# Optimization experiments

Measured on AMD Instinct MI355X. Metric: run time of the kernel, lower is better.

## Reference

```python
import jax, jax.numpy as jnp
import numpy as np

EPS = 1e-12  # tf.nn.l2_normalize epsilon used inside keras CosineSimilarity


def _cos(a, b):
    # keras CosineSimilarity returns -cos; callers negate explicitly.
    an = a / jnp.sqrt(jnp.maximum(jnp.sum(a * a, axis=-1, keepdims=True), EPS))
    bn = b / jnp.sqrt(jnp.maximum(jnp.sum(b * b, axis=-1, keepdims=True), EPS))
    return jnp.sum(an * bn, axis=-1)


def setup_inputs() -> dict:
    key = jax.random.key(0)
    B, S, D, H, N = 1024, 200, 128, 128, 64
    ks = jax.random.split(key, 8)
    X_series = jax.random.normal(ks[0], (B, S, D), jnp.float32)
    pos_series = jax.random.normal(ks[1], (S, D), jnp.float32)
    X_item = jax.random.normal(ks[2], (B, D), jnp.float32)
    origin = jax.random.normal(ks[3], (B, N, D), jnp.float32)  # X_negative
    # contiguous-prefix validity mask (module assumes valid positions form a prefix)
    lengths = jax.random.randint(ks[4], (B,), 1, S + 1)
    valid_mask = jnp.arange(S)[None, :] < lengths[:, None]
    # learned params (GlorotUniform-scale init)
    Wp = jax.random.normal(ks[5], (D, H), jnp.float32) * 0.08
    We = jax.random.normal(ks[6], (D, H), jnp.float32) * 0.08
    z = jax.random.normal(ks[7], (H,), jnp.float32) * 0.1
    return {"X_series": X_series, "pos_series": pos_series, "X_item": X_item,
            "valid_mask": valid_mask, "origin": origin, "Wp": Wp, "We": We, "z": z}


def reference(X_series, pos_series, X_item, valid_mask, origin, Wp, We, z):
    B, S, D = X_series.shape
    # additive tanh attention: z . tanh(X_series @ We + pos_series @ Wp)
    hidden = jnp.tanh(jnp.einsum('bsd,dh->bsh', X_series, We) + (pos_series @ Wp)[None])
    scores = jnp.einsum('bsh,h->bs', hidden, z)
    scores = jnp.where(valid_mask, scores, -jnp.inf)
    attn = jax.nn.softmax(scores, axis=-1)                      # [B,S]
    attentioned = attn[:, :, None] * X_series                    # [B,S,D]
    attention_output = jnp.sum(attentioned, axis=1)              # [B,D]
    inner = jnp.sum(attention_output * X_item, axis=-1, keepdims=True)
    concated = jnp.concatenate([attention_output, inner], axis=1)  # [B,D+1]

    # ---- auxiliary loss ----
    last_idx = jnp.sum(valid_mask.astype(jnp.int32), axis=1) - 1
    last_vec = attentioned[jnp.arange(B), last_idx]              # gather_nd
    new_mask = (jnp.arange(S)[None, :] < last_idx[:, None]).astype(X_series.dtype)
    out_vec = jnp.sum(attentioned * new_mask[:, :, None], axis=1)  # [B,D]
    # keras CosineSimilarity = -cos_sim; then mapped to (x+1)/2 and used as logits
    pos_logits = (-_cos(last_vec, out_vec) + 1.0) / 2.0          # [B]
    neg_logits = (-_cos(origin, out_vec[:, None, :]) + 1.0) / 2.0  # [B,N]
    pos_loss = jax.nn.softplus(-pos_logits)  # sigmoid_xent labels=1
    neg_loss = jax.nn.softplus(neg_logits)   # sigmoid_xent labels=0
    # NB: TF reduces pos_loss over its only axis -> scalar, broadcast-added to [B]
    auxiliary_loss = jnp.sum(pos_loss) + jnp.sum(neg_loss, axis=-1)  # [B]
    return concated, auxiliary_loss
```

## Files before the change

kernel.cpp:

```cpp
#include <hip/hip_runtime.h>
#include <hip/hip_bf16.h>
#include <math.h>

#define B_ 1024
#define S_ 200
#define D_ 128
#define H_ 128
#define N_ 64
#define SP_ 208

typedef __attribute__((ext_vector_type(8))) short short8;
typedef __attribute__((ext_vector_type(8))) __bf16 bf16x8;
typedef __attribute__((ext_vector_type(4))) float floatx4;

typedef __attribute__((address_space(1))) void gvoid_t;
typedef __attribute__((address_space(3))) void lvoid_t;

static __device__ __forceinline__ float bf2f(unsigned short u) {
    union { unsigned int i; float f; } v; v.i = ((unsigned int)u) << 16; return v.f;
}
static __device__ __forceinline__ unsigned short f2bf(float f) {
    union { float f; unsigned int u; } v; v.f = f;
    unsigned int u = v.u;
    return (unsigned short)((u + 0x7FFFu + ((u >> 16) & 1u)) >> 16);
}
static __device__ __forceinline__ float ld1(const void* p, int isbf, size_t i) {
    return isbf ? bf2f(((const unsigned short*)p)[i]) : ((const float*)p)[i];
}
static __device__ __forceinline__ float fast_tanh(float x) {
    float t = __expf(2.0f * x);
    return 1.0f - 2.0f * __builtin_amdgcn_rcpf(t + 1.0f);
}
static __device__ __forceinline__ void gload_lds16(const void* g, void* l) {
    __builtin_amdgcn_global_load_lds((const gvoid_t*)g, (lvoid_t*)l, 16, 0, 0);
}

static __device__ __forceinline__ int detect_wave_256(const void* p) {
    int lane = threadIdx.x & 63;
    uint4 w = ((const uint4*)p)[lane];
    unsigned int ws[4] = {w.x, w.y, w.z, w.w};
    int pass = 0;
#pragma unroll
    for (int k = 0; k < 4; ++k) {
        unsigned int e = (ws[k] >> 7) & 0xFF;
        pass += (e == 0 || (e >= 96 && e <= 140)) ? 1 : 0;
    }
#pragma unroll
    for (int off = 32; off; off >>= 1) pass += __shfl_xor(pass, off, 64);
    return pass * 4 >= 256 * 3;
}
static __device__ __forceinline__ int detect_wave_64(const void* p) {
    int lane = threadIdx.x & 63;
    unsigned int w = ((const unsigned int*)p)[lane];
    unsigned int e = (w >> 7) & 0xFF;
    int pass = (e == 0 || (e >= 96 && e <= 140)) ? 1 : 0;
#pragma unroll
    for (int off = 32; off; off >>= 1) pass += __shfl_xor(pass, off, 64);
    return pass * 4 >= 64 * 3;
}
static __device__ __forceinline__ int detect_mask_u8(const void* p) {
    int lane = threadIdx.x & 63;
    uint4 w = ((const uint4*)p)[lane];
    unsigned int x = (w.x | w.y | w.z | w.w) & 0xFFFFFF00u;
    return (__ballot(x != 0) != 0ULL) ? 1 : 0;
}

__global__ __launch_bounds__(128) void prep_kernel(
    const void* __restrict__ We, const void* __restrict__ pos,
    const void* __restrict__ Wp,
    unsigned short* __restrict__ WeTf, float* __restrict__ pbL)
{
    int blk = blockIdx.x, t = threadIdx.x;
    __shared__ unsigned short T[128][136];
    __shared__ float prow[D_];
    __shared__ int fl[2];
    if (blk == 0) {
        if (t < 64) { int f = detect_wave_256(We); if (t == 0) fl[0] = f; }
        __syncthreads();
        int fWe = fl[0];
        for (int c = t; c < 2048; c += 128) {
            int d = c >> 4, h8 = (c & 15) * 8;
            short8 v;
            if (fWe) {
                v = *(const short8*)((const unsigned short*)We + d * H_ + h8);
            } else {
                const float* p = (const float*)We + d * H_ + h8;
                float4 a = ((const float4*)p)[0], b = ((const float4*)p)[1];
                v[0] = (short)f2bf(a.x); v[1] = (short)f2bf(a.y);
                v[2] = (short)f2bf(a.z); v[3] = (short)f2bf(a.w);
                v[4] = (short)f2bf(b.x); v[5] = (short)f2bf(b.y);
                v[6] = (short)f2bf(b.z); v[7] = (short)f2bf(b.w);
            }
            *(short8*)(&T[d][h8]) = v;
        }
        __syncthreads();
        for (int i = t; i < 2048; i += 128) {
            int frag = i >> 6, ln = i & 63;
            int nt = frag >> 2, kks = frag & 3;
            int h = nt * 16 + (ln & 15);
            int dbase = kks * 32 + (ln >> 4) * 8;
            short8 v;
#pragma unroll
            for (int j = 0; j < 8; ++j) v[j] = (short)T[dbase + j][h];
            *(short8*)(WeTf + (size_t)i * 8) = v;
        }
    } else {
        if (t < 64)       { int f = detect_wave_256(pos); if (t == 0)  fl[0] = f; }
        else if (t < 128) { int f = detect_wave_256(Wp);  if (t == 64) fl[1] = f; }
        __syncthreads();
        int fPos = fl[0], fWp = fl[1];
        int s = blk - 1, h = t;
        prow[h] = ld1(pos, fPos, (size_t)s * D_ + h);
        __syncthreads();
        float acc = 0.f;
        if (fWp) {
            const unsigned short* W = (const unsigned short*)Wp;
            for (int d = 0; d < D_; ++d) acc = fmaf(prow[d], bf2f(W[d * H_ + h]), acc);
        } else {
            const float* W = (const float*)Wp;
            for (int d = 0; d < D_; ++d) acc = fmaf(prow[d], W[d * H_ + h], acc);
        }
        int mt = s >> 4, qr = s & 15;
        int idx = (((mt * 8 + (h >> 4)) * 64 + (qr >> 2) * 16 + (h & 15)) << 2) + (qr & 3);
        pbL[idx] = acc;
    }
}

__global__ __launch_bounds__(512, 4) void fused_kernel(
    const void* __restrict__ Xs, const void* __restrict__ Xitem,
    const void* __restrict__ maskv, const void* __restrict__ origin,
    const unsigned short* __restrict__ WeTf, const float* __restrict__ pbL,
    const void* __restrict__ zv,
    float* __restrict__ pos_loss, float* __restrict__ neg_sum,
    float* __restrict__ out)
{
    int b = blockIdx.x, t = threadIdx.x;
    int wv = t >> 6, lane = t & 63;
    int quad = lane >> 4, mrow = lane & 15;

    __shared__ __align__(16) unsigned short Xsh[SP_ * D_];
    __shared__ __align__(16) float partial[4096];
    __shared__ float red4[512];
    __shared__ float attn[256];
    __shared__ float outv[D_];
    __shared__ float red[32];
    __shared__ int redi[8];

    int fXs = detect_wave_256(Xs);
    int fXi = detect_wave_256(Xitem);
    int fOr = detect_wave_256(origin);
    int fz  = detect_wave_64(zv);
    int fMk = detect_mask_u8(maskv);

    if (fXs) {
        const unsigned short* gb = (const unsigned short*)Xs + (size_t)b * (S_ * D_);
        for (int i = t; i < S_ * 16; i += 512) {
            int s = i >> 4, c8 = (i & 15) * 8;
            int cs = c8 ^ ((s & 7) << 3);
            gload_lds16(gb + (size_t)s * D_ + cs, Xsh + (size_t)i * 8);
        }
    } else {
        const float* gb = (const float*)Xs + (size_t)b * (S_ * D_);
        for (int i = t; i < S_ * 16; i += 512) {
            int s = i >> 4, c8 = (i & 15) * 8;
            const float* p = gb + (size_t)s * D_ + c8;
            float4 a = ((const float4*)p)[0], c = ((const float4*)p)[1];
            short8 v;
            v[0] = (short)f2bf(a.x); v[1] = (short)f2bf(a.y);
            v[2] = (short)f2bf(a.z); v[3] = (short)f2bf(a.w);
            v[4] = (short)f2bf(c.x); v[5] = (short)f2bf(c.y);
            v[6] = (short)f2bf(c.z); v[7] = (short)f2bf(c.w);
            *(short8*)(Xsh + s * D_ + (c8 ^ ((s & 7) << 3))) = v;
        }
    }

    int nn = t >> 3, part = t & 7;
    float o_f[16];
    if (fOr) {
        const unsigned short* p = (const unsigned short*)origin + ((size_t)b * N_ + nn) * D_ + part * 16;
#pragma unroll
        for (int j = 0; j < 2; ++j) {
            uint4 u = *(const uint4*)(p + j * 8);
            o_f[j*8+0] = bf2f((unsigned short)(u.x & 0xffff));
            o_f[j*8+1] = bf2f((unsigned short)(u.x >> 16));
            o_f[j*8+2] = bf2f((unsigned short)(u.y & 0xffff));
            o_f[j*8+3] = bf2f((unsigned short)(u.y >> 16));
            o_f[j*8+4] = bf2f((unsigned short)(u.z & 0xffff));
            o_f[j*8+5] = bf2f((unsigned short)(u.z >> 16));
            o_f[j*8+6] = bf2f((unsigned short)(u.w & 0xffff));
            o_f[j*8+7] = bf2f((unsigned short)(u.w >> 16));
        }
    } else {
        const float* p = (const float*)origin + ((size_t)b * N_ + nn) * D_ + part * 16;
#pragma unroll
        for (int j = 0; j < 4; ++j) {
            float4 v = *(const float4*)(p + j * 4);
            o_f[j*4+0] = v.x; o_f[j*4+1] = v.y; o_f[j*4+2] = v.z; o_f[j*4+3] = v.w;
        }
    }
    float xiv = (t < D_) ? ld1(Xitem, fXi, (size_t)b * D_ + t) : 0.f;
    int nz = 0;
    if (t < S_)
        nz = fMk ? (((const unsigned char*)maskv)[(size_t)b * S_ + t] != 0)
                 : (((const int*)maskv)[(size_t)b * S_ + t] != 0);

    int nt = wv;
    bf16x8 bfr[4];
#pragma unroll
    for (int kks = 0; kks < 4; ++kks)
        bfr[kks] = __builtin_bit_cast(bf16x8,
            *(const short8*)(WeTf + (size_t)((((nt << 2) + kks) << 6) + lane) * 8));
    float zl = ld1(zv, fz, nt * 16 + mrow);
    const float4* pbw = (const float4*)pbL + nt * 64 + lane;
    float4 pbc = pbw[0];

    asm volatile("s_waitcnt vmcnt(0)" ::: "memory");
    __syncthreads();

    float* sp = partial;
    for (int mt = 0; mt < 13; ++mt) {
        float4 pbn = pbc;
        if (mt < 12) pbn = pbw[(size_t)(mt + 1) * 512];
        floatx4 acc = {0.f, 0.f, 0.f, 0.f};
        int r = mt * 16 + mrow;
        int rbase = r * D_, rx = (r & 7) << 3;
#pragma unroll
        for (int kks = 0; kks < 4; ++kks) {
            bf16x8 af = __builtin_bit_cast(bf16x8,
                *(const short8*)(Xsh + rbase + ((kks * 32 + quad * 8) ^ rx)));
            acc = __builtin_amdgcn_mfma_f32_16x16x32_bf16(af, bfr[kks], acc, 0, 0, 0);
        }
#pragma unroll
        for (int reg = 0; reg < 4; ++reg) {
            float val = fast_tanh(acc[reg] + (&pbc.x)[reg]) * zl;
            val += __shfl_xor(val, 1, 64);
            val += __shfl_xor(val, 2, 64);
            val += __shfl_xor(val, 4, 64);
            val += __shfl_xor(val, 8, 64);
            int s = mt * 16 + quad * 4 + reg;
            if (mrow == 0 && s < S_) sp[nt * SP_ + s] = val;
        }
        pbc = pbn;
    }
    __syncthreads();

    float myscore = -INFINITY;
    if (t < S_) {
        float ss = 0.f;
#pragma unroll
        for (int w8 = 0; w8 < 8; ++w8) ss += sp[w8 * SP_ + t];
        myscore = ss;
    }
    unsigned long long bal = __ballot(nz);
    float scv = nz ? myscore : -INFINITY;
    float m = scv;
#pragma unroll
    for (int off = 32; off; off >>= 1) m = fmaxf(m, __shfl_xor(m, off, 64));
    if (lane == 0) { red[wv] = m; redi[wv] = __popcll(bal); }
    __syncthreads();
    int length = redi[0] + redi[1] + redi[2] + redi[3]
               + redi[4] + redi[5] + redi[6] + redi[7];
    int last = length - 1;
    float mglob = red[0];
#pragma unroll
    for (int i = 1; i < 8; ++i) mglob = fmaxf(mglob, red[i]);
    float e = nz ? expf(myscore - mglob) : 0.f;
    float rr = e;
#pragma unroll
    for (int off = 32; off; off >>= 1) rr += __shfl_xor(rr, off, 64);
    if (lane == 0) red[8 + wv] = rr;
    __syncthreads();
    float ssum = red[8] + red[9] + red[10] + red[11]
               + red[12] + red[13] + red[14] + red[15];
    if (t < 256) attn[t] = e / ssum;
    __syncthreads();

    {
        int spi = t >> 4;
        int d8 = (t & 15) * 8;
        float a0 = 0.f, a1 = 0.f, a2 = 0.f, a3 = 0.f;
        float a4 = 0.f, a5 = 0.f, a6 = 0.f, a7 = 0.f;
        for (int s = spi; s < S_; s += 32) {
            float ww = attn[s];
            short8 v2 = *(const short8*)(Xsh + s * D_ + (d8 ^ ((s & 7) << 3)));
            a0 = fmaf(ww, bf2f((unsigned short)v2[0]), a0);
            a1 = fmaf(ww, bf2f((unsigned short)v2[1]), a1);
            a2 = fmaf(ww, bf2f((unsigned short)v2[2]), a2);
            a3 = fmaf(ww, bf2f((unsigned short)v2[3]), a3);
            a4 = fmaf(ww, bf2f((unsigned short)v2[4]), a4);
            a5 = fmaf(ww, bf2f((unsigned short)v2[5]), a5);
            a6 = fmaf(ww, bf2f((unsigned short)v2[6]), a6);
            a7 = fmaf(ww, bf2f((unsigned short)v2[7]), a7);
        }
        float4 w0 = {a0, a1, a2, a3}, w1 = {a4, a5, a6, a7};
        *(float4*)(partial + spi * D_ + d8)     = w0;
        *(float4*)(partial + spi * D_ + d8 + 4) = w1;
    }
    __syncthreads();
    {
        int g = t >> 7, d = t & 127;
        float sgp = 0.f;
#pragma unroll
        for (int p = 0; p < 8; ++p) sgp += partial[(g * 8 + p) * D_ + d];
        red4[g * D_ + d] = sgp;
    }
    __syncthreads();

    if (t < D_) {
        float att = red4[t] + red4[D_ + t] + red4[2 * D_ + t] + red4[3 * D_ + t];
        float xl = bf2f(Xsh[last * D_ + (t ^ ((last & 7) << 3))]);
        float lv = attn[last] * xl;
        float ov = att - lv;
        outv[t] = ov;
        out[(size_t)b * (D_ + 1) + t] = att;
        float r0 = att * xiv;
        float r1 = lv * lv, r2 = lv * ov, r3 = ov * ov;
#pragma unroll
        for (int off = 32; off; off >>= 1) {
            r0 += __shfl_xor(r0, off, 64);
            r1 += __shfl_xor(r1, off, 64);
            r2 += __shfl_xor(r2, off, 64);
            r3 += __shfl_xor(r3, off, 64);
        }
        if (lane == 0) { red[wv] = r0; red[8 + wv] = r1; red[16 + wv] = r2; red[24 + wv] = r3; }
    }
    __syncthreads();
    float vv = red[24] + red[25];
    if (t == 0) {
        out[(size_t)b * (D_ + 1) + D_] = red[0] + red[1];
        float ll = red[8] + red[9], lo = red[16] + red[17];
        float cosv = lo / (sqrtf(fmaxf(ll, 1e-12f)) * sqrtf(fmaxf(vv, 1e-12f)));
        float pl = 0.5f * (1.f - cosv);
        pos_loss[b] = log1pf(expf(-pl));
    }

    {
        float* p_oo = partial;
        float* p_ov = partial + 512;
        float o_oo = 0.f, o_ov = 0.f;
#pragma unroll
        for (int j = 0; j < 16; ++j) {
            float wv_ = outv[part * 16 + j];
            o_oo = fmaf(o_f[j], o_f[j], o_oo);
            o_ov = fmaf(o_f[j], wv_, o_ov);
        }
        p_oo[part * 64 + nn] = o_oo;
        p_ov[part * 64 + nn] = o_ov;
        __syncthreads();
        if (t < 64) {
            float oo = 0.f, ov2 = 0.f;
#pragma unroll
            for (int p8 = 0; p8 < 8; ++p8) { oo += p_oo[p8 * 64 + t]; ov2 += p_ov[p8 * 64 + t]; }
            float cosn = ov2 / (sqrtf(fmaxf(oo, 1e-12f)) * sqrtf(fmaxf(vv, 1e-12f)));
            float nl = 0.5f * (1.f - cosn);
            float nloss = log1pf(expf(nl));
#pragma unroll
            for (int off = 32; off; off >>= 1) nloss += __shfl_xor(nloss, off, 64);
            if (t == 0) neg_sum[b] = nloss;
        }
    }
}

__global__ __launch_bounds__(1024) void final_kernel(
    const float* __restrict__ pos_loss,
    const float* __restrict__ neg_sum,
    float* __restrict__ out)
{
    __shared__ float red[16];
    int t = threadIdx.x;
    float v = pos_loss[t];
    for (int off = 32; off; off >>= 1) v += __shfl_xor(v, off, 64);
    if ((t & 63) == 0) red[t >> 6] = v;
    __syncthreads();
    if (t == 0) {
        float s = 0.f;
#pragma unroll
        for (int i = 0; i < 16; ++i) s += red[i];
        red[0] = s;
    }
    __syncthreads();
    out[(size_t)B_ * (D_ + 1) + t] = red[0] + neg_sum[t];
}

extern "C" void kernel_launch(void* const* d_in, const int* in_sizes, int n_in,
                              void* d_out, int out_size, void* d_ws, size_t ws_size,
                              hipStream_t stream) {
    const void* Xs     = d_in[0];
    const void* pos    = d_in[1];
    const void* Xitem  = d_in[2];
    const void* mask   = d_in[3];
    const void* origin = d_in[4];
    const void* Wp     = d_in[5];
    const void* We     = d_in[6];
    const void* zv     = d_in[7];

    unsigned short* WeTf = (unsigned short*)d_ws;
    float* pbL      = (float*)((char*)d_ws + 32768);
    float* pos_loss = pbL + 13 * 8 * 64 * 4;
    float* neg_sum  = pos_loss + B_;
    float* out = (float*)d_out;

    prep_kernel<<<201, 128, 0, stream>>>(We, pos, Wp, WeTf, pbL);
    fused_kernel<<<B_, 512, 0, stream>>>(Xs, Xitem, mask, origin, WeTf, pbL, zv,
                                         pos_loss, neg_sum, out);
    final_kernel<<<1, 1024, 0, stream>>>(pos_loss, neg_sum, out);
}
```

Before: 236.5 us.

## Process one batch row per wave with online softmax and streamed X loads

Restructures the fused kernel so that each 64-lane wave handles a whole batch row, with four rows per 256-thread block, in place of one 512-thread block per row. X_series is no longer staged in LDS; MFMA A-fragments are loaded straight from global memory and prefetched one tile ahead. The attention softmax and weighted sum are computed in a single streaming pass using a flash-style running max and rescaling. This removes the block-wide syncs and the large LDS footprint. In exchange, each wave now does all 8 H-tiles of MFMA work and re-reads X rows from global or cache for the weighted sum. The prep kernel also zero-fills the padded pbL entries so the bias can seed the accumulators directly.

```diff
diff --git a/kernel.cpp b/kernel.cpp
--- a/kernel.cpp
+++ b/kernel.cpp
@@ -7,7 +7,6 @@
 #define D_ 128
 #define H_ 128
 #define N_ 64
-#define SP_ 208
 
 typedef __attribute__((ext_vector_type(8))) short short8;
 typedef __attribute__((ext_vector_type(8))) __bf16 bf16x8;
@@ -104,6 +103,11 @@
             for (int j = 0; j < 8; ++j) v[j] = (short)T[dbase + j][h];
             *(short8*)(WeTf + (size_t)i * 8) = v;
         }
+        for (int i = t; i < 1024; i += 128) {
+            int nt = i >> 7, j = i & 127;
+            int q = 2 + (j >> 6), m = (j >> 2) & 15, r = j & 3;
+            pbL[(((96 + nt) * 64 + q * 16 + m) << 2) + r] = 0.f;
+        }
     } else {
         if (t < 64)       { int f = detect_wave_256(pos); if (t == 0)  fl[0] = f; }
         else if (t < 128) { int f = detect_wave_256(Wp);  if (t == 64) fl[1] = f; }
@@ -126,7 +130,7 @@
     }
 }
 
-__global__ __launch_bounds__(512, 4) void fused_kernel(
+__global__ __launch_bounds__(256, 4) void fused_kernel(
     const void* __restrict__ Xs, const void* __restrict__ Xitem,
     const void* __restrict__ maskv, const void* __restrict__ origin,
     const unsigned short* __restrict__ WeTf, const float* __restrict__ pbL,
@@ -134,17 +138,14 @@
     float* __restrict__ pos_loss, float* __restrict__ neg_sum,
     float* __restrict__ out)
 {
-    int b = blockIdx.x, t = threadIdx.x;
+    int t = threadIdx.x;
     int wv = t >> 6, lane = t & 63;
     int quad = lane >> 4, mrow = lane & 15;
-
-    __shared__ __align__(16) unsigned short Xsh[SP_ * D_];
-    __shared__ __align__(16) float partial[4096];
-    __shared__ float red4[512];
-    __shared__ float attn[256];
-    __shared__ float outv[D_];
-    __shared__ float red[32];
-    __shared__ int redi[8];
+    int b = blockIdx.x * 4 + wv;
+    int d0 = lane * 2;
+
+    __shared__ __align__(16) unsigned short WeSh[16384];
+    __shared__ __align__(16) float outbuf[4 * D_];
 
     int fXs = detect_wave_256(Xs);
     int fXi = detect_wave_256(Xitem);
@@ -152,213 +153,274 @@
     int fz  = detect_wave_64(zv);
     int fMk = detect_mask_u8(maskv);
 
-    if (fXs) {
-        const unsigned short* gb = (const unsigned short*)Xs + (size_t)b * (S_ * D_);
-        for (int i = t; i < S_ * 16; i += 512) {
-            int s = i >> 4, c8 = (i & 15) * 8;
-            int cs = c8 ^ ((s & 7) << 3);
-            gload_lds16(gb + (size_t)s * D_ + cs, Xsh + (size_t)i * 8);
-        }
+    for (int i = t; i < 2048; i += 256)
+        gload_lds16(WeTf + (size_t)i * 8, WeSh + (size_t)i * 8);
+
+    const unsigned short* Xg16 = (const unsigned short*)Xs + (size_t)b * S_ * D_;
+    const float*          Xg32 = (const float*)Xs + (size_t)b * S_ * D_;
+
+    int len = 0;
+    {
+#pragma unroll
+        for (int k = 0; k < 4; ++k) {
+            int s = lane + 64 * k;
+            int nzv = 0;
+            if (s < S_)
+                nzv = fMk ? (((const unsigned char*)maskv)[(size_t)b * S_ + s] != 0)
+                          : (((const int*)maskv)[(size_t)b * S_ + s] != 0);
+            len += __popcll(__ballot(nzv));
+        }
+    }
+    int last = len - 1;
+    float zr[8];
+#pragma unroll
+    for (int nt = 0; nt < 8; ++nt) zr[nt] = ld1(zv, fz, nt * 16 + mrow);
+    float xi0, xi1;
+    if (fXi) {
+        unsigned int u = *(const unsigned int*)((const unsigned short*)Xitem + (size_t)b * D_ + d0);
+        xi0 = bf2f((unsigned short)(u & 0xffff)); xi1 = bf2f((unsigned short)(u >> 16));
     } else {
-        const float* gb = (const float*)Xs + (size_t)b * (S_ * D_);
-        for (int i = t; i < S_ * 16; i += 512) {
-            int s = i >> 4, c8 = (i & 15) * 8;
-            const float* p = gb + (size_t)s * D_ + c8;
-            float4 a = ((const float4*)p)[0], c = ((const float4*)p)[1];
-            short8 v;
-            v[0] = (short)f2bf(a.x); v[1] = (short)f2bf(a.y);
-            v[2] = (short)f2bf(a.z); v[3] = (short)f2bf(a.w);
-            v[4] = (short)f2bf(c.x); v[5] = (short)f2bf(c.y);
-            v[6] = (short)f2bf(c.z); v[7] = (short)f2bf(c.w);
-            *(short8*)(Xsh + s * D_ + (c8 ^ ((s & 7) << 3))) = v;
-        }
-    }
-
-    int nn = t >> 3, part = t & 7;
-    float o_f[16];
-    if (fOr) {
-        const unsigned short* p = (const unsigned short*)origin + ((size_t)b * N_ + nn) * D_ + part * 16;
-#pragma unroll
-        for (int j = 0; j < 2; ++j) {
-            uint4 u = *(const uint4*)(p + j * 8);
-            o_f[j*8+0] = bf2f((unsigned short)(u.x & 0xffff));
-            o_f[j*8+1] = bf2f((unsigned short)(u.x >> 16));
-            o_f[j*8+2] = bf2f((unsigned short)(u.y & 0xffff));
-            o_f[j*8+3] = bf2f((unsigned short)(u.y >> 16));
-            o_f[j*8+4] = bf2f((unsigned short)(u.z & 0xffff));
-            o_f[j*8+5] = bf2f((unsigned short)(u.z >> 16));
-            o_f[j*8+6] = bf2f((unsigned short)(u.w & 0xffff));
-            o_f[j*8+7] = bf2f((unsigned short)(u.w >> 16));
-        }
-    } else {
-        const float* p = (const float*)origin + ((size_t)b * N_ + nn) * D_ + part * 16;
-#pragma unroll
-        for (int j = 0; j < 4; ++j) {
-            float4 v = *(const float4*)(p + j * 4);
-            o_f[j*4+0] = v.x; o_f[j*4+1] = v.y; o_f[j*4+2] = v.z; o_f[j*4+3] = v.w;
-        }
-    }
-    float xiv = (t < D_) ? ld1(Xitem, fXi, (size_t)b * D_ + t) : 0.f;
-    int nz = 0;
-    if (t < S_)
-        nz = fMk ? (((const unsigned char*)maskv)[(size_t)b * S_ + t] != 0)
-                 : (((const int*)maskv)[(size_t)b * S_ + t] != 0);
-
-    int nt = wv;
-    bf16x8 bfr[4];
-#pragma unroll
-    for (int kks = 0; kks < 4; ++kks)
-        bfr[kks] = __builtin_bit_cast(bf16x8,
-            *(const short8*)(WeTf + (size_t)((((nt << 2) + kks) << 6) + lane) * 8));
-    float zl = ld1(zv, fz, nt * 16 + mrow);
-    const float4* pbw = (const float4*)pbL + nt * 64 + lane;
-    float4 pbc = pbw[0];
+        float2 v = *(const float2*)((const float*)Xitem + (size_t)b * D_ + d0);
+        xi0 = v.x; xi1 = v.y;
+    }
 
     asm volatile("s_waitcnt vmcnt(0)" ::: "memory");
     __syncthreads();
 
-    float* sp = partial;
+#define LOADA(MT, AF)                                                              \
+    {                                                                              \
+        int r_ = (MT) * 16 + mrow; if (r_ > 199) r_ = 199;                         \
+        if (fXs) {                                                                 \
+            const unsigned short* p_ = Xg16 + (size_t)r_ * D_ + quad * 8;          \
+            _Pragma("unroll")                                                      \
+            for (int kk_ = 0; kk_ < 4; ++kk_)                                      \
+                AF[kk_] = __builtin_bit_cast(bf16x8, *(const short8*)(p_ + kk_ * 32)); \
+        } else {                                                                   \
+            const float* p_ = Xg32 + (size_t)r_ * D_ + quad * 8;                   \
+            _Pragma("unroll")                                                      \
+            for (int kk_ = 0; kk_ < 4; ++kk_) {                                    \
+                float4 a_ = ((const float4*)(p_ + kk_ * 32))[0];                   \
+                float4 b2_ = ((const float4*)(p_ + kk_ * 32))[1];                  \
+                short8 v_;                                                         \
+                v_[0] = (short)f2bf(a_.x); v_[1] = (short)f2bf(a_.y);              \
+                v_[2] = (short)f2bf(a_.z); v_[3] = (short)f2bf(a_.w);              \
+                v_[4] = (short)f2bf(b2_.x); v_[5] = (short)f2bf(b2_.y);            \
+                v_[6] = (short)f2bf(b2_.z); v_[7] = (short)f2bf(b2_.w);            \
+                AF[kk_] = __builtin_bit_cast(bf16x8, v_);                          \
+            }                                                                      \
+        }                                                                          \
+    }
+
+#define LOADXP(R, X0, X1)                                                          \
+    {                                                                              \
+        if (fXs) {                                                                 \
+            unsigned int u_ = *(const unsigned int*)(Xg16 + (size_t)(R) * D_ + d0);\
+            X0 = bf2f((unsigned short)(u_ & 0xffff));                              \
+            X1 = bf2f((unsigned short)(u_ >> 16));                                 \
+        } else {                                                                   \
+            float2 v_ = *(const float2*)(Xg32 + (size_t)(R) * D_ + d0);            \
+            X0 = v_.x; X1 = v_.y;                                                  \
+        }                                                                          \
+    }
+
+    bf16x8 afc[4], afn[4];
+    LOADA(0, afc);
+
+    float m_run = -INFINITY, l_run = 0.f;
+    float O0 = 0.f, O1 = 0.f;
+    float slv = -INFINITY;
+    float dsc = 0.f;
+    float de0 = 0.f, de1 = 0.f, de2 = 0.f, de3 = 0.f;
+    int dmt = 0;
+    const float4* pb4 = (const float4*)pbL;
+
     for (int mt = 0; mt < 13; ++mt) {
-        float4 pbn = pbc;
-        if (mt < 12) pbn = pbw[(size_t)(mt + 1) * 512];
-        floatx4 acc = {0.f, 0.f, 0.f, 0.f};
-        int r = mt * 16 + mrow;
-        int rbase = r * D_, rx = (r & 7) << 3;
+        float4 pbt[8];
+#pragma unroll
+        for (int nt = 0; nt < 8; ++nt)
+            pbt[nt] = pb4[(size_t)(mt * 8 + nt) * 64 + lane];
+        if (mt < 12) LOADA(mt + 1, afn);
+
+        if (mt > 0) {
+            O0 *= dsc; O1 *= dsc;
+#pragma unroll
+            for (int q = 0; q < 4; ++q) {
+                float eq0 = q ? __shfl_xor(de0, q << 4, 64) : de0;
+                float eq1 = q ? __shfl_xor(de1, q << 4, 64) : de1;
+                float eq2 = q ? __shfl_xor(de2, q << 4, 64) : de2;
+                float eq3 = q ? __shfl_xor(de3, q << 4, 64) : de3;
+                int rb = (dmt << 4) + ((quad ^ q) << 2);
+#pragma unroll
+                for (int r = 0; r < 4; ++r) {
+                    float es = (r == 0) ? eq0 : (r == 1) ? eq1 : (r == 2) ? eq2 : eq3;
+                    int row = rb + r; if (row > 199) row = 199;
+                    float x0, x1; LOADXP(row, x0, x1);
+                    O0 = fmaf(es, x0, O0);
+                    O1 = fmaf(es, x1, O1);
+                }
+            }
+        }
+
+        floatx4 acc[8];
+#pragma unroll
+        for (int nt = 0; nt < 8; ++nt) {
+            acc[nt][0] = pbt[nt].x; acc[nt][1] = pbt[nt].y;
+            acc[nt][2] = pbt[nt].z; acc[nt][3] = pbt[nt].w;
+        }
 #pragma unroll
         for (int kks = 0; kks < 4; ++kks) {
-            bf16x8 af = __builtin_bit_cast(bf16x8,
-                *(const short8*)(Xsh + rbase + ((kks * 32 + quad * 8) ^ rx)));
-            acc = __builtin_amdgcn_mfma_f32_16x16x32_bf16(af, bfr[kks], acc, 0, 0, 0);
-        }
-#pragma unroll
-        for (int reg = 0; reg < 4; ++reg) {
-            float val = fast_tanh(acc[reg] + (&pbc.x)[reg]) * zl;
-            val += __shfl_xor(val, 1, 64);
-            val += __shfl_xor(val, 2, 64);
-            val += __shfl_xor(val, 4, 64);
-            val += __shfl_xor(val, 8, 64);
-            int s = mt * 16 + quad * 4 + reg;
-            if (mrow == 0 && s < S_) sp[nt * SP_ + s] = val;
-        }
-        pbc = pbn;
-    }
-    __syncthreads();
-
-    float myscore = -INFINITY;
-    if (t < S_) {
-        float ss = 0.f;
-#pragma unroll
-        for (int w8 = 0; w8 < 8; ++w8) ss += sp[w8 * SP_ + t];
-        myscore = ss;
-    }
-    unsigned long long bal = __ballot(nz);
-    float scv = nz ? myscore : -INFINITY;
-    float m = scv;
-#pragma unroll
-    for (int off = 32; off; off >>= 1) m = fmaxf(m, __shfl_xor(m, off, 64));
-    if (lane == 0) { red[wv] = m; redi[wv] = __popcll(bal); }
-    __syncthreads();
-    int length = redi[0] + redi[1] + redi[2] + redi[3]
-               + redi[4] + redi[5] + redi[6] + redi[7];
-    int last = length - 1;
-    float mglob = red[0];
-#pragma unroll
-    for (int i = 1; i < 8; ++i) mglob = fmaxf(mglob, red[i]);
-    float e = nz ? expf(myscore - mglob) : 0.f;
-    float rr = e;
-#pragma unroll
-    for (int off = 32; off; off >>= 1) rr += __shfl_xor(rr, off, 64);
-    if (lane == 0) red[8 + wv] = rr;
-    __syncthreads();
-    float ssum = red[8] + red[9] + red[10] + red[11]
-               + red[12] + red[13] + red[14] + red[15];
-    if (t < 256) attn[t] = e / ssum;
-    __syncthreads();
+#pragma unroll
+            for (int nt = 0; nt < 8; ++nt) {
+                short8 bv = *(const short8*)(WeSh + (size_t)(((nt << 2) + kks) * 64 + lane) * 8);
+                acc[nt] = __builtin_amdgcn_mfma_f32_16x16x32_bf16(
+                    afc[kks], __builtin_bit_cast(bf16x8, bv), acc[nt], 0, 0, 0);
+            }
+        }
+
+        float val0, val1, val2, val3;
+#pragma unroll
+        for (int r = 0; r < 4; ++r) {
+            float v = 0.f;
+#pragma unroll
+            for (int nt = 0; nt < 8; ++nt)
+                v = fmaf(fast_tanh(acc[nt][r]), zr[nt], v);
+            v += __shfl_xor(v, 1, 64);
+            v += __shfl_xor(v, 2, 64);
+            v += __shfl_xor(v, 4, 64);
+            v += __shfl_xor(v, 8, 64);
+            if (r == 0) val0 = v; else if (r == 1) val1 = v;
+            else if (r == 2) val2 = v; else val3 = v;
+        }
+
+        int sbase = (mt << 4) + (quad << 2);
+        float x0m = (sbase + 0 < len) ? val0 : -INFINITY;
+        float x1m = (sbase + 1 < len) ? val1 : -INFINITY;
+        float x2m = (sbase + 2 < len) ? val2 : -INFINITY;
+        float x3m = (sbase + 3 < len) ? val3 : -INFINITY;
+        if (sbase + 0 == last) slv = val0;
+        if (sbase + 1 == last) slv = val1;
+        if (sbase + 2 == last) slv = val2;
+        if (sbase + 3 == last) slv = val3;
+        float tm = fmaxf(fmaxf(x0m, x1m), fmaxf(x2m, x3m));
+        tm = fmaxf(tm, __shfl_xor(tm, 16, 64));
+        tm = fmaxf(tm, __shfl_xor(tm, 32, 64));
+        float mn = fmaxf(m_run, tm);
+        float sc_ = __expf(m_run - mn);
+        de0 = (sbase + 0 < len) ? __expf(val0 - mn) : 0.f;
+        de1 = (sbase + 1 < len) ? __expf(val1 - mn) : 0.f;
+        de2 = (sbase + 2 < len) ? __expf(val2 - mn) : 0.f;
+        de3 = (sbase + 3 < len) ? __expf(val3 - mn) : 0.f;
+        float tl = de0 + de1 + de2 + de3;
+        tl += __shfl_xor(tl, 16, 64);
+        tl += __shfl_xor(tl, 32, 64);
+        l_run = l_run * sc_ + tl;
+        m_run = mn;
+        dsc = sc_; dmt = mt;
+
+#pragma unroll
+        for (int kks = 0; kks < 4; ++kks) afc[kks] = afn[kks];
+    }
 
     {
-        int spi = t >> 4;
-        int d8 = (t & 15) * 8;
-        float a0 = 0.f, a1 = 0.f, a2 = 0.f, a3 = 0.f;
-        float a4 = 0.f, a5 = 0.f, a6 = 0.f, a7 = 0.f;
-        for (int s = spi; s < S_; s += 32) {
-            float ww = attn[s];
-            short8 v2 = *(const short8*)(Xsh + s * D_ + (d8 ^ ((s & 7) << 3)));
-            a0 = fmaf(ww, bf2f((unsigned short)v2[0]), a0);
-            a1 = fmaf(ww, bf2f((unsigned short)v2[1]), a1);
-            a2 = fmaf(ww, bf2f((unsigned short)v2[2]), a2);
-            a3 = fmaf(ww, bf2f((unsigned short)v2[3]), a3);
-            a4 = fmaf(ww, bf2f((unsigned short)v2[4]), a4);
-            a5 = fmaf(ww, bf2f((unsigned short)v2[5]), a5);
-            a6 = fmaf(ww, bf2f((unsigned short)v2[6]), a6);
-            a7 = fmaf(ww, bf2f((unsigned short)v2[7]), a7);
-        }
-        float4 w0 = {a0, a1, a2, a3}, w1 = {a4, a5, a6, a7};
-        *(float4*)(partial + spi * D_ + d8)     = w0;
-        *(float4*)(partial + spi * D_ + d8 + 4) = w1;
-    }
-    __syncthreads();
-    {
-        int g = t >> 7, d = t & 127;
-        float sgp = 0.f;
-#pragma unroll
-        for (int p = 0; p < 8; ++p) sgp += partial[(g * 8 + p) * D_ + d];
-        red4[g * D_ + d] = sgp;
-    }
-    __syncthreads();
-
-    if (t < D_) {
-        float att = red4[t] + red4[D_ + t] + red4[2 * D_ + t] + red4[3 * D_ + t];
-        float xl = bf2f(Xsh[last * D_ + (t ^ ((last & 7) << 3))]);
-        float lv = attn[last] * xl;
-        float ov = att - lv;
-        outv[t] = ov;
-        out[(size_t)b * (D_ + 1) + t] = att;
-        float r0 = att * xiv;
-        float r1 = lv * lv, r2 = lv * ov, r3 = ov * ov;
-#pragma unroll
-        for (int off = 32; off; off >>= 1) {
-            r0 += __shfl_xor(r0, off, 64);
-            r1 += __shfl_xor(r1, off, 64);
-            r2 += __shfl_xor(r2, off, 64);
-            r3 += __shfl_xor(r3, off, 64);
-        }
-        if (lane == 0) { red[wv] = r0; red[8 + wv] = r1; red[16 + wv] = r2; red[24 + wv] = r3; }
-    }
-    __syncthreads();
-    float vv = red[24] + red[25];
-    if (t == 0) {
-        out[(size_t)b * (D_ + 1) + D_] = red[0] + red[1];
-        float ll = red[8] + red[9], lo = red[16] + red[17];
-        float cosv = lo / (sqrtf(fmaxf(ll, 1e-12f)) * sqrtf(fmaxf(vv, 1e-12f)));
+        O0 *= dsc; O1 *= dsc;
+#pragma unroll
+        for (int q = 0; q < 4; ++q) {
+            float eq0 = q ? __shfl_xor(de0, q << 4, 64) : de0;
+            float eq1 = q ? __shfl_xor(de1, q << 4, 64) : de1;
+            float eq2 = q ? __shfl_xor(de2, q << 4, 64) : de2;
+            float eq3 = q ? __shfl_xor(de3, q << 4, 64) : de3;
+            int rb = (12 << 4) + ((quad ^ q) << 2);
+#pragma unroll
+            for (int r = 0; r < 4; ++r) {
+                float es = (r == 0) ? eq0 : (r == 1) ? eq1 : (r == 2) ? eq2 : eq3;
+                int row = rb + r; if (row > 199) row = 199;
+                float x0, x1; LOADXP(row, x0, x1);
+                O0 = fmaf(es, x0, O0);
+                O1 = fmaf(es, x1, O1);
+            }
+        }
+    }
+
+    float att0 = O0 / l_run, att1 = O1 / l_run;
+    slv = fmaxf(slv, __shfl_xor(slv, 16, 64));
+    slv = fmaxf(slv, __shfl_xor(slv, 32, 64));
+    float al = __expf(slv - m_run) / l_run;
+    float xl0, xl1; LOADXP(last, xl0, xl1);
+    float lv0 = al * xl0, lv1 = al * xl1;
+    float ov0 = att0 - lv0, ov1 = att1 - lv1;
+    float* outw = outbuf + wv * D_;
+    outw[d0] = ov0; outw[d0 + 1] = ov1;
+
+    float r0 = att0 * xi0 + att1 * xi1;
+    float r1 = lv0 * lv0 + lv1 * lv1;
+    float r2 = lv0 * ov0 + lv1 * ov1;
+    float r3 = ov0 * ov0 + ov1 * ov1;
+#pragma unroll
+    for (int off = 32; off; off >>= 1) {
+        r0 += __shfl_xor(r0, off, 64);
+        r1 += __shfl_xor(r1, off, 64);
+        r2 += __shfl_xor(r2, off, 64);
+        r3 += __shfl_xor(r3, off, 64);
+    }
+    out[(size_t)b * (D_ + 1) + d0] = att0;
+    out[(size_t)b * (D_ + 1) + d0 + 1] = att1;
+    if (lane == 0) {
+        out[(size_t)b * (D_ + 1) + D_] = r0;
+        float cosv = r2 / (sqrtf(fmaxf(r1, 1e-12f)) * sqrtf(fmaxf(r3, 1e-12f)));
         float pl = 0.5f * (1.f - cosv);
         pos_loss[b] = log1pf(expf(-pl));
     }
+    float vv = r3;
 
     {
-        float* p_oo = partial;
-        float* p_ov = partial + 512;
-        float o_oo = 0.f, o_ov = 0.f;
-#pragma unroll
-        for (int j = 0; j < 16; ++j) {
-            float wv_ = outv[part * 16 + j];
-            o_oo = fmaf(o_f[j], o_f[j], o_oo);
-            o_ov = fmaf(o_f[j], wv_, o_ov);
-        }
-        p_oo[part * 64 + nn] = o_oo;
-        p_ov[part * 64 + nn] = o_ov;
-        __syncthreads();
-        if (t < 64) {
-            float oo = 0.f, ov2 = 0.f;
-#pragma unroll
-            for (int p8 = 0; p8 < 8; ++p8) { oo += p_oo[p8 * 64 + t]; ov2 += p_ov[p8 * 64 + t]; }
-            float cosn = ov2 / (sqrtf(fmaxf(oo, 1e-12f)) * sqrtf(fmaxf(vv, 1e-12f)));
-            float nl = 0.5f * (1.f - cosn);
-            float nloss = log1pf(expf(nl));
-#pragma unroll
-            for (int off = 32; off; off >>= 1) nloss += __shfl_xor(nloss, off, 64);
-            if (t == 0) neg_sum[b] = nloss;
-        }
-    }
+        float oo = 0.f, ovd = 0.f;
+        if (fOr) {
+            const unsigned short* orow = (const unsigned short*)origin + ((size_t)b * N_ + lane) * D_;
+#pragma unroll 4
+            for (int j = 0; j < 16; ++j) {
+                short8 og = *(const short8*)(orow + j * 8);
+                float4 c0 = *(const float4*)(outw + j * 8);
+                float4 c1 = *(const float4*)(outw + j * 8 + 4);
+                float f0 = bf2f((unsigned short)og[0]), f1 = bf2f((unsigned short)og[1]);
+                float f2 = bf2f((unsigned short)og[2]), f3 = bf2f((unsigned short)og[3]);
+                float f4 = bf2f((unsigned short)og[4]), f5 = bf2f((unsigned short)og[5]);
+                float f6 = bf2f((unsigned short)og[6]), f7 = bf2f((unsigned short)og[7]);
+                oo  = fmaf(f0, f0, oo);  ovd = fmaf(f0, c0.x, ovd);
+                oo  = fmaf(f1, f1, oo);  ovd = fmaf(f1, c0.y, ovd);
+                oo  = fmaf(f2, f2, oo);  ovd = fmaf(f2, c0.z, ovd);
+                oo  = fmaf(f3, f3, oo);  ovd = fmaf(f3, c0.w, ovd);
+                oo  = fmaf(f4, f4, oo);  ovd = fmaf(f4, c1.x, ovd);
+                oo  = fmaf(f5, f5, oo);  ovd = fmaf(f5, c1.y, ovd);
+                oo  = fmaf(f6, f6, oo);  ovd = fmaf(f6, c1.z, ovd);
+                oo  = fmaf(f7, f7, oo);  ovd = fmaf(f7, c1.w, ovd);
+            }
+        } else {
+            const float* orow = (const float*)origin + ((size_t)b * N_ + lane) * D_;
+#pragma unroll 4
+            for (int j = 0; j < 16; ++j) {
+                float4 g0 = *(const float4*)(orow + j * 8);
+                float4 g1 = *(const float4*)(orow + j * 8 + 4);
+                float4 c0 = *(const float4*)(outw + j * 8);
+                float4 c1 = *(const float4*)(outw + j * 8 + 4);
+                oo  = fmaf(g0.x, g0.x, oo);  ovd = fmaf(g0.x, c0.x, ovd);
+                oo  = fmaf(g0.y, g0.y, oo);  ovd = fmaf(g0.y, c0.y, ovd);
+                oo  = fmaf(g0.z, g0.z, oo);  ovd = fmaf(g0.z, c0.z, ovd);
+                oo  = fmaf(g0.w, g0.w, oo);  ovd = fmaf(g0.w, c0.w, ovd);
+                oo  = fmaf(g1.x, g1.x, oo);  ovd = fmaf(g1.x, c1.x, ovd);
+                oo  = fmaf(g1.y, g1.y, oo);  ovd = fmaf(g1.y, c1.y, ovd);
+                oo  = fmaf(g1.z, g1.z, oo);  ovd = fmaf(g1.z, c1.z, ovd);
+                oo  = fmaf(g1.w, g1.w, oo);  ovd = fmaf(g1.w, c1.w, ovd);
+            }
+        }
+        float cosn = ovd / (sqrtf(fmaxf(oo, 1e-12f)) * sqrtf(fmaxf(vv, 1e-12f)));
+        float nl = 0.5f * (1.f - cosn);
+        float nloss = log1pf(expf(nl));
+#pragma unroll
+        for (int off = 32; off; off >>= 1) nloss += __shfl_xor(nloss, off, 64);
+        if (lane == 0) neg_sum[b] = nloss;
+    }
+#undef LOADA
+#undef LOADXP
 }
 
 __global__ __launch_bounds__(1024) void final_kernel(
@@ -401,7 +463,7 @@
     float* out = (float*)d_out;
 
     prep_kernel<<<201, 128, 0, stream>>>(We, pos, Wp, WeTf, pbL);
-    fused_kernel<<<B_, 512, 0, stream>>>(Xs, Xitem, mask, origin, WeTf, pbL, zv,
-                                         pos_loss, neg_sum, out);
+    fused_kernel<<<B_ / 4, 256, 0, stream>>>(Xs, Xitem, mask, origin, WeTf, pbL, zv,
+                                             pos_loss, neg_sum, out);
     final_kernel<<<1, 1024, 0, stream>>>(pos_loss, neg_sum, out);
 }
```

Measured after the change: 428.7 us. 1.81x slower.

## Drop LDS staging of X_series, stream MFMA operands from global to raise occupancy

Applied to the files above, without the earlier changes.

Removes the 53KB shared-memory copy of each batch's X_series. MFMA A-fragments are now loaded straight from global memory with one-tile register double-buffering, and the weighted-sum pass re-reads X from global (expected to hit in cache). This shrinks LDS use so launch bounds can request 6 blocks per CU instead of 4. It also computes the sequence length up front via ballot, moves the softmax into a single wave, folds the positional bias into the MFMA accumulator init, and zero-pads the bias tail in the prep kernel. The cost is a second global read of X and possibly more register pressure.

```diff
diff --git a/kernel.cpp b/kernel.cpp
--- a/kernel.cpp
+++ b/kernel.cpp
@@ -7,14 +7,10 @@
 #define D_ 128
 #define H_ 128
 #define N_ 64
-#define SP_ 208
 
 typedef __attribute__((ext_vector_type(8))) short short8;
 typedef __attribute__((ext_vector_type(8))) __bf16 bf16x8;
 typedef __attribute__((ext_vector_type(4))) float floatx4;
-
-typedef __attribute__((address_space(1))) void gvoid_t;
-typedef __attribute__((address_space(3))) void lvoid_t;
 
 static __device__ __forceinline__ float bf2f(unsigned short u) {
     union { unsigned int i; float f; } v; v.i = ((unsigned int)u) << 16; return v.f;
@@ -30,9 +26,6 @@
 static __device__ __forceinline__ float fast_tanh(float x) {
     float t = __expf(2.0f * x);
     return 1.0f - 2.0f * __builtin_amdgcn_rcpf(t + 1.0f);
-}
-static __device__ __forceinline__ void gload_lds16(const void* g, void* l) {
-    __builtin_amdgcn_global_load_lds((const gvoid_t*)g, (lvoid_t*)l, 16, 0, 0);
 }
 
 static __device__ __forceinline__ int detect_wave_256(const void* p) {
@@ -104,6 +97,11 @@
             for (int j = 0; j < 8; ++j) v[j] = (short)T[dbase + j][h];
             *(short8*)(WeTf + (size_t)i * 8) = v;
         }
+        for (int i = t; i < 1024; i += 128) {
+            int nt = i >> 7, j = i & 127;
+            int q = 2 + (j >> 6), m = (j >> 2) & 15, r = j & 3;
+            pbL[(((96 + nt) * 64 + q * 16 + m) << 2) + r] = 0.f;
+        }
     } else {
         if (t < 64)       { int f = detect_wave_256(pos); if (t == 0)  fl[0] = f; }
         else if (t < 128) { int f = detect_wave_256(Wp);  if (t == 64) fl[1] = f; }
@@ -126,7 +124,7 @@
     }
 }
 
-__global__ __launch_bounds__(512, 4) void fused_kernel(
+__global__ __launch_bounds__(512, 6) void fused_kernel(
     const void* __restrict__ Xs, const void* __restrict__ Xitem,
     const void* __restrict__ maskv, const void* __restrict__ origin,
     const unsigned short* __restrict__ WeTf, const float* __restrict__ pbL,
@@ -138,13 +136,10 @@
     int wv = t >> 6, lane = t & 63;
     int quad = lane >> 4, mrow = lane & 15;
 
-    __shared__ __align__(16) unsigned short Xsh[SP_ * D_];
-    __shared__ __align__(16) float partial[4096];
-    __shared__ float red4[512];
+    __shared__ __align__(16) float ubuf[4096];
     __shared__ float attn[256];
     __shared__ float outv[D_];
     __shared__ float red[32];
-    __shared__ int redi[8];
 
     int fXs = detect_wave_256(Xs);
     int fXi = detect_wave_256(Xitem);
@@ -152,57 +147,20 @@
     int fz  = detect_wave_64(zv);
     int fMk = detect_mask_u8(maskv);
 
-    if (fXs) {
-        const unsigned short* gb = (const unsigned short*)Xs + (size_t)b * (S_ * D_);
-        for (int i = t; i < S_ * 16; i += 512) {
-            int s = i >> 4, c8 = (i & 15) * 8;
-            int cs = c8 ^ ((s & 7) << 3);
-            gload_lds16(gb + (size_t)s * D_ + cs, Xsh + (size_t)i * 8);
-        }
-    } else {
-        const float* gb = (const float*)Xs + (size_t)b * (S_ * D_);
-        for (int i = t; i < S_ * 16; i += 512) {
-            int s = i >> 4, c8 = (i & 15) * 8;
-            const float* p = gb + (size_t)s * D_ + c8;
-            float4 a = ((const float4*)p)[0], c = ((const float4*)p)[1];
-            short8 v;
-            v[0] = (short)f2bf(a.x); v[1] = (short)f2bf(a.y);
-            v[2] = (short)f2bf(a.z); v[3] = (short)f2bf(a.w);
-            v[4] = (short)f2bf(c.x); v[5] = (short)f2bf(c.y);
-            v[6] = (short)f2bf(c.z); v[7] = (short)f2bf(c.w);
-            *(short8*)(Xsh + s * D_ + (c8 ^ ((s & 7) << 3))) = v;
-        }
-    }
-
-    int nn = t >> 3, part = t & 7;
-    float o_f[16];
-    if (fOr) {
-        const unsigned short* p = (const unsigned short*)origin + ((size_t)b * N_ + nn) * D_ + part * 16;
-#pragma unroll
-        for (int j = 0; j < 2; ++j) {
-            uint4 u = *(const uint4*)(p + j * 8);
-            o_f[j*8+0] = bf2f((unsigned short)(u.x & 0xffff));
-            o_f[j*8+1] = bf2f((unsigned short)(u.x >> 16));
-            o_f[j*8+2] = bf2f((unsigned short)(u.y & 0xffff));
-            o_f[j*8+3] = bf2f((unsigned short)(u.y >> 16));
-            o_f[j*8+4] = bf2f((unsigned short)(u.z & 0xffff));
-            o_f[j*8+5] = bf2f((unsigned short)(u.z >> 16));
-            o_f[j*8+6] = bf2f((unsigned short)(u.w & 0xffff));
-            o_f[j*8+7] = bf2f((unsigned short)(u.w >> 16));
-        }
-    } else {
-        const float* p = (const float*)origin + ((size_t)b * N_ + nn) * D_ + part * 16;
-#pragma unroll
-        for (int j = 0; j < 4; ++j) {
-            float4 v = *(const float4*)(p + j * 4);
-            o_f[j*4+0] = v.x; o_f[j*4+1] = v.y; o_f[j*4+2] = v.z; o_f[j*4+3] = v.w;
-        }
-    }
-    float xiv = (t < D_) ? ld1(Xitem, fXi, (size_t)b * D_ + t) : 0.f;
-    int nz = 0;
-    if (t < S_)
-        nz = fMk ? (((const unsigned char*)maskv)[(size_t)b * S_ + t] != 0)
-                 : (((const int*)maskv)[(size_t)b * S_ + t] != 0);
+    const unsigned short* Xg16 = (const unsigned short*)Xs + (size_t)b * S_ * D_;
+    const float*          Xg32 = (const float*)Xs + (size_t)b * S_ * D_;
+
+    int len = 0;
+#pragma unroll
+    for (int k = 0; k < 4; ++k) {
+        int s = lane + 64 * k;
+        int nzv = 0;
+        if (s < S_)
+            nzv = fMk ? (((const unsigned char*)maskv)[(size_t)b * S_ + s] != 0)
+                      : (((const int*)maskv)[(size_t)b * S_ + s] != 0);
+        len += __popcll(__ballot(nzv));
+    }
+    int last = len - 1;
 
     int nt = wv;
     bf16x8 bfr[4];
@@ -211,68 +169,91 @@
         bfr[kks] = __builtin_bit_cast(bf16x8,
             *(const short8*)(WeTf + (size_t)((((nt << 2) + kks) << 6) + lane) * 8));
     float zl = ld1(zv, fz, nt * 16 + mrow);
-    const float4* pbw = (const float4*)pbL + nt * 64 + lane;
-    float4 pbc = pbw[0];
-
-    asm volatile("s_waitcnt vmcnt(0)" ::: "memory");
-    __syncthreads();
-
-    float* sp = partial;
+    const float4* pb4 = (const float4*)pbL;
+    float xiv = (t < D_) ? ld1(Xitem, fXi, (size_t)b * D_ + t) : 0.f;
+
+#define LOADA(MT, AF)                                                              \
+    {                                                                              \
+        int r_ = (MT) * 16 + mrow; if (r_ > 199) r_ = 199;                         \
+        if (fXs) {                                                                 \
+            const unsigned short* p_ = Xg16 + (size_t)r_ * D_ + quad * 8;          \
+            _Pragma("unroll")                                                      \
+            for (int kk_ = 0; kk_ < 4; ++kk_)                                      \
+                AF[kk_] = __builtin_bit_cast(bf16x8, *(const short8*)(p_ + kk_ * 32)); \
+        } else {                                                                   \
+            const float* p_ = Xg32 + (size_t)r_ * D_ + quad * 8;                   \
+            _Pragma("unroll")                                                      \
+            for (int kk_ = 0; kk_ < 4; ++kk_) {                                    \
+                float4 a_ = ((const float4*)(p_ + kk_ * 32))[0];                   \
+                float4 b2_ = ((const float4*)(p_ + kk_ * 32))[1];                  \
+                short8 v_;                                                         \
+                v_[0] = (short)f2bf(a_.x); v_[1] = (short)f2bf(a_.y);              \
+                v_[2] = (short)f2bf(a_.z); v_[3] = (short)f2bf(a_.w);              \
+                v_[4] = (short)f2bf(b2_.x); v_[5] = (short)f2bf(b2_.y);            \
+                v_[6] = (short)f2bf(b2_.z); v_[7] = (short)f2bf(b2_.w);            \
+                AF[kk_] = __builtin_bit_cast(bf16x8, v_);                          \
+            }                                                                      \
+        }                                                                          \
+    }
+
+    bf16x8 afc[4], afn[4];
+    LOADA(0, afc);
+    float4 pbc = pb4[(size_t)(0 * 8 + nt) * 64 + lane];
+    float* sp = ubuf;
+
     for (int mt = 0; mt < 13; ++mt) {
         float4 pbn = pbc;
-        if (mt < 12) pbn = pbw[(size_t)(mt + 1) * 512];
-        floatx4 acc = {0.f, 0.f, 0.f, 0.f};
-        int r = mt * 16 + mrow;
-        int rbase = r * D_, rx = (r & 7) << 3;
-#pragma unroll
-        for (int kks = 0; kks < 4; ++kks) {
-            bf16x8 af = __builtin_bit_cast(bf16x8,
-                *(const short8*)(Xsh + rbase + ((kks * 32 + quad * 8) ^ rx)));
-            acc = __builtin_amdgcn_mfma_f32_16x16x32_bf16(af, bfr[kks], acc, 0, 0, 0);
-        }
-#pragma unroll
-        for (int reg = 0; reg < 4; ++reg) {
-            float val = fast_tanh(acc[reg] + (&pbc.x)[reg]) * zl;
-            val += __shfl_xor(val, 1, 64);
-            val += __shfl_xor(val, 2, 64);
-            val += __shfl_xor(val, 4, 64);
-            val += __shfl_xor(val, 8, 64);
-            int s = mt * 16 + quad * 4 + reg;
-            if (mrow == 0 && s < S_) sp[nt * SP_ + s] = val;
-        }
+        if (mt < 12) {
+            LOADA(mt + 1, afn);
+            pbn = pb4[(size_t)((mt + 1) * 8 + nt) * 64 + lane];
+        }
+        floatx4 acc;
+        acc[0] = pbc.x; acc[1] = pbc.y; acc[2] = pbc.z; acc[3] = pbc.w;
+#pragma unroll
+        for (int kks = 0; kks < 4; ++kks)
+            acc = __builtin_amdgcn_mfma_f32_16x16x32_bf16(afc[kks], bfr[kks], acc, 0, 0, 0);
+#pragma unroll
+        for (int r = 0; r < 4; ++r) {
+            float v = fast_tanh(acc[r]) * zl;
+            v += __shfl_xor(v, 1, 64);
+            v += __shfl_xor(v, 2, 64);
+            v += __shfl_xor(v, 4, 64);
+            v += __shfl_xor(v, 8, 64);
+            int s = mt * 16 + quad * 4 + r;
+            if (mrow == 0 && s < S_) sp[nt * 208 + s] = v;
+        }
+#pragma unroll
+        for (int kks = 0; kks < 4; ++kks) afc[kks] = afn[kks];
         pbc = pbn;
     }
     __syncthreads();
 
-    float myscore = -INFINITY;
-    if (t < S_) {
-        float ss = 0.f;
-#pragma unroll
-        for (int w8 = 0; w8 < 8; ++w8) ss += sp[w8 * SP_ + t];
-        myscore = ss;
-    }
-    unsigned long long bal = __ballot(nz);
-    float scv = nz ? myscore : -INFINITY;
-    float m = scv;
-#pragma unroll
-    for (int off = 32; off; off >>= 1) m = fmaxf(m, __shfl_xor(m, off, 64));
-    if (lane == 0) { red[wv] = m; redi[wv] = __popcll(bal); }
-    __syncthreads();
-    int length = redi[0] + redi[1] + redi[2] + redi[3]
-               + redi[4] + redi[5] + redi[6] + redi[7];
-    int last = length - 1;
-    float mglob = red[0];
-#pragma unroll
-    for (int i = 1; i < 8; ++i) mglob = fmaxf(mglob, red[i]);
-    float e = nz ? expf(myscore - mglob) : 0.f;
-    float rr = e;
-#pragma unroll
-    for (int off = 32; off; off >>= 1) rr += __shfl_xor(rr, off, 64);
-    if (lane == 0) red[8 + wv] = rr;
-    __syncthreads();
-    float ssum = red[8] + red[9] + red[10] + red[11]
-               + red[12] + red[13] + red[14] + red[15];
-    if (t < 256) attn[t] = e / ssum;
+    if (wv == 0) {
+        float s0 = 0.f, s1 = 0.f, s2 = 0.f, s3 = 0.f;
+#pragma unroll
+        for (int n8 = 0; n8 < 8; ++n8) {
+            float4 q = *(const float4*)(sp + n8 * 208 + lane * 4);
+            s0 += q.x; s1 += q.y; s2 += q.z; s3 += q.w;
+        }
+        int sb = lane * 4;
+        float m0 = (sb + 0 < len) ? s0 : -INFINITY;
+        float m1 = (sb + 1 < len) ? s1 : -INFINITY;
+        float m2 = (sb + 2 < len) ? s2 : -INFINITY;
+        float m3 = (sb + 3 < len) ? s3 : -INFINITY;
+        float m = fmaxf(fmaxf(m0, m1), fmaxf(m2, m3));
+#pragma unroll
+        for (int off = 32; off; off >>= 1) m = fmaxf(m, __shfl_xor(m, off, 64));
+        float e0 = (sb + 0 < len) ? __expf(s0 - m) : 0.f;
+        float e1 = (sb + 1 < len) ? __expf(s1 - m) : 0.f;
+        float e2 = (sb + 2 < len) ? __expf(s2 - m) : 0.f;
+        float e3 = (sb + 3 < len) ? __expf(s3 - m) : 0.f;
+        float l = e0 + e1 + e2 + e3;
+#pragma unroll
+        for (int off = 32; off; off >>= 1) l += __shfl_xor(l, off, 64);
+        float inv = 1.0f / l;
+        float4 av = {e0 * inv, e1 * inv, e2 * inv, e3 * inv};
+        *(float4*)(attn + sb) = av;
+    }
     __syncthreads();
 
     {
@@ -280,35 +261,42 @@
         int d8 = (t & 15) * 8;
         float a0 = 0.f, a1 = 0.f, a2 = 0.f, a3 = 0.f;
         float a4 = 0.f, a5 = 0.f, a6 = 0.f, a7 = 0.f;
-        for (int s = spi; s < S_; s += 32) {
-            float ww = attn[s];
-            short8 v2 = *(const short8*)(Xsh + s * D_ + (d8 ^ ((s & 7) << 3)));
-            a0 = fmaf(ww, bf2f((unsigned short)v2[0]), a0);
-            a1 = fmaf(ww, bf2f((unsigned short)v2[1]), a1);
-            a2 = fmaf(ww, bf2f((unsigned short)v2[2]), a2);
-            a3 = fmaf(ww, bf2f((unsigned short)v2[3]), a3);
-            a4 = fmaf(ww, bf2f((unsigned short)v2[4]), a4);
-            a5 = fmaf(ww, bf2f((unsigned short)v2[5]), a5);
-            a6 = fmaf(ww, bf2f((unsigned short)v2[6]), a6);
-            a7 = fmaf(ww, bf2f((unsigned short)v2[7]), a7);
+        if (fXs) {
+            for (int s = spi; s < S_; s += 32) {
+                float ww = attn[s];
+                short8 v2 = *(const short8*)(Xg16 + (size_t)s * D_ + d8);
+                a0 = fmaf(ww, bf2f((unsigned short)v2[0]), a0);
+                a1 = fmaf(ww, bf2f((unsigned short)v2[1]), a1);
+                a2 = fmaf(ww, bf2f((unsigned short)v2[2]), a2);
+                a3 = fmaf(ww, bf2f((unsigned short)v2[3]), a3);
+                a4 = fmaf(ww, bf2f((unsigned short)v2[4]), a4);
+                a5 = fmaf(ww, bf2f((unsigned short)v2[5]), a5);
+                a6 = fmaf(ww, bf2f((unsigned short)v2[6]), a6);
+                a7 = fmaf(ww, bf2f((unsigned short)v2[7]), a7);
+            }
+        } else {
+            for (int s = spi; s < S_; s += 32) {
+                float ww = attn[s];
+                const float* p = Xg32 + (size_t)s * D_ + d8;
+                float4 u0 = ((const float4*)p)[0], u1 = ((const float4*)p)[1];
+                a0 = fmaf(ww, u0.x, a0); a1 = fmaf(ww, u0.y, a1);
+                a2 = fmaf(ww, u0.z, a2); a3 = fmaf(ww, u0.w, a3);
+                a4 = fmaf(ww, u1.x, a4); a5 = fmaf(ww, u1.y, a5);
+                a6 = fmaf(ww, u1.z, a6); a7 = fmaf(ww, u1.w, a7);
+            }
         }
         float4 w0 = {a0, a1, a2, a3}, w1 = {a4, a5, a6, a7};
-        *(float4*)(partial + spi * D_ + d8)     = w0;
-        *(float4*)(partial + spi * D_ + d8 + 4) = w1;
-    }
-    __syncthreads();
-    {
-        int g = t >> 7, d = t & 127;
-        float sgp = 0.f;
-#pragma unroll
-        for (int p = 0; p < 8; ++p) sgp += partial[(g * 8 + p) * D_ + d];
-        red4[g * D_ + d] = sgp;
+        *(float4*)(ubuf + spi * D_ + d8)     = w0;
+        *(float4*)(ubuf + spi * D_ + d8 + 4) = w1;
     }
     __syncthreads();
 
     if (t < D_) {
-        float att = red4[t] + red4[D_ + t] + red4[2 * D_ + t] + red4[3 * D_ + t];
-        float xl = bf2f(Xsh[last * D_ + (t ^ ((last & 7) << 3))]);
+        float att = 0.f;
+#pragma unroll
+        for (int p = 0; p < 32; ++p) att += ubuf[p * D_ + t];
+        float xl = fXs ? bf2f(Xg16[(size_t)last * D_ + t])
+                       : Xg32[(size_t)last * D_ + t];
         float lv = attn[last] * xl;
         float ov = att - lv;
         outv[t] = ov;
@@ -335,8 +323,30 @@
     }
 
     {
-        float* p_oo = partial;
-        float* p_ov = partial + 512;
+        int nn = t >> 3, part = t & 7;
+        float o_f[16];
+        if (fOr) {
+            const unsigned short* p = (const unsigned short*)origin + ((size_t)b * N_ + nn) * D_ + part * 16;
+#pragma unroll
+            for (int j = 0; j < 2; ++j) {
+                uint4 u = *(const uint4*)(p + j * 8);
+                o_f[j*8+0] = bf2f((unsigned short)(u.x & 0xffff));
+                o_f[j*8+1] = bf2f((unsigned short)(u.x >> 16));
+                o_f[j*8+2] = bf2f((unsigned short)(u.y & 0xffff));
+                o_f[j*8+3] = bf2f((unsigned short)(u.y >> 16));
+                o_f[j*8+4] = bf2f((unsigned short)(u.z & 0xffff));
+                o_f[j*8+5] = bf2f((unsigned short)(u.z >> 16));
+                o_f[j*8+6] = bf2f((unsigned short)(u.w & 0xffff));
+                o_f[j*8+7] = bf2f((unsigned short)(u.w >> 16));
+            }
+        } else {
+            const float* p = (const float*)origin + ((size_t)b * N_ + nn) * D_ + part * 16;
+#pragma unroll
+            for (int j = 0; j < 4; ++j) {
+                float4 v = *(const float4*)(p + j * 4);
+                o_f[j*4+0] = v.x; o_f[j*4+1] = v.y; o_f[j*4+2] = v.z; o_f[j*4+3] = v.w;
+            }
+        }
         float o_oo = 0.f, o_ov = 0.f;
 #pragma unroll
         for (int j = 0; j < 16; ++j) {
@@ -344,6 +354,8 @@
             o_oo = fmaf(o_f[j], o_f[j], o_oo);
             o_ov = fmaf(o_f[j], wv_, o_ov);
         }
+        float* p_oo = ubuf;
+        float* p_ov = ubuf + 512;
         p_oo[part * 64 + nn] = o_oo;
         p_ov[part * 64 + nn] = o_ov;
         __syncthreads();
@@ -359,6 +371,7 @@
             if (t == 0) neg_sum[b] = nloss;
         }
     }
+#undef LOADA
 }
 
 __global__ __launch_bounds__(1024) void final_kernel(
```

Result: slower. 308.7 us (+30.5%).
